# Kernel optimization log

Hardware: AMD Instinct MI355X
Metric: run time of the kernel (lower is better)

## Reference

```python
import jax, jax.numpy as jnp
import numpy as np

B, T, N_EMBD, N_HEAD = 2, 2048, 1024, 16
HEAD = N_EMBD // N_HEAD  # 64
BLOCK = 2048             # config.block_size
BASE = 10000.0           # RoPE base


def rotate_half(x):
    h = x.shape[-1] // 2
    return jnp.concatenate([-x[..., h:], x[..., :h]], axis=-1)


def setup_inputs() -> dict:
    key = jax.random.key(0)
    ks = jax.random.split(key, 6)
    x = jax.random.normal(ks[0], (B, T, N_EMBD), jnp.float32)
    cumulative_scores = jax.random.uniform(ks[1], (B, T), jnp.float32)
    token_index = jnp.sort(jax.random.randint(ks[2], (B, T), 0, BLOCK), axis=-1)
    padding_mask = jnp.ones((B, BLOCK), jnp.float32)
    W_attn = jax.random.normal(ks[3], (N_EMBD, 3 * N_EMBD), jnp.float32) * 0.02
    b_attn = jnp.zeros((3 * N_EMBD,), jnp.float32)
    W_proj = jax.random.normal(ks[4], (N_EMBD, N_EMBD), jnp.float32) * 0.02
    b_proj = jnp.zeros((N_EMBD,), jnp.float32)
    return {"x": x, "cumulative_scores": cumulative_scores,
            "padding_mask": padding_mask, "W_attn": W_attn, "b_attn": b_attn,
            "W_proj": W_proj, "b_proj": b_proj, "token_index": token_index}


def reference(x, cumulative_scores, padding_mask, W_attn, b_attn, W_proj, b_proj, token_index):
    Bv, Tv, C = x.shape
    qkv = x @ W_attn + b_attn                      # [B,T,3C]
    q, k, v = jnp.split(qkv, 3, axis=-1)
    to_heads = lambda a: a.reshape(Bv, Tv, N_HEAD, HEAD).transpose(0, 2, 1, 3)  # [B,H,T,hd]
    q, k, v = to_heads(q), to_heads(k), to_heads(v)

    # per-token fractional positions: cumsum of 1/count over gathered token indices
    counts = jax.vmap(lambda idx: jnp.zeros(BLOCK, jnp.float32).at[idx].add(1.0))(token_index)
    partial = jnp.cumsum(jnp.take_along_axis(1.0 / counts, token_index, axis=-1), axis=-1)  # [B,T]

    # RoPE with custom positions t=partial
    inv_freq = 1.0 / (BASE ** (jnp.arange(0, HEAD, 2, dtype=jnp.float32) / HEAD))  # [hd/2]
    freqs = partial[..., None] * inv_freq                                          # [B,T,hd/2]
    emb = jnp.concatenate([freqs, freqs], axis=-1)[:, None, :, :]                  # [B,1,T,hd]
    cos, sin = jnp.cos(emb), jnp.sin(emb)
    q = q * cos + rotate_half(q) * sin
    k = k * cos + rotate_half(k) * sin

    # 'fork' plan: overwrite last channel
    q = q.at[..., -1].set(1.0)
    k = k.at[..., -1].set(jnp.broadcast_to(cumulative_scores[:, None, :], k.shape[:-1]))

    # additive bf16 causal + padding mask, then cast to q dtype
    zero_bf = jnp.zeros((), jnp.bfloat16)
    neg_bf = jnp.full((), -jnp.inf, jnp.bfloat16)
    causal = jnp.where(jnp.tril(jnp.ones((Tv, Tv), bool)), zero_bf, neg_bf)        # [T,T] bf16
    pm = jnp.take_along_axis(padding_mask, token_index, axis=1).astype(jnp.float32)  # [B,T]
    outer = pm[:, :, None] * pm[:, None, :]                                        # [B,T,T]
    pad_add = jnp.where(outer != 0, zero_bf, neg_bf)
    mask = (causal[None] + pad_add).astype(x.dtype)[:, None, :, :]                 # [B,1,T,T]

    # scale v by exp(cumulative_scores)
    v = v * jnp.exp(cumulative_scores)[:, None, :, None]

    scores = jnp.einsum('bhqd,bhkd->bhqk', q, k) / np.float32(np.sqrt(HEAD)) + mask
    p = jax.nn.softmax(scores, axis=-1)
    y = jnp.einsum('bhqk,bhkd->bhqd', p, v)
    y = y.transpose(0, 2, 1, 3).reshape(Bv, Tv, C)
    return y @ W_proj + b_proj
```

## Files before the change

### kernel.cpp

```cpp
#include <hip/hip_runtime.h>
#include <math.h>

#define B_ 2
#define T_ 2048
#define C_ 1024
#define H_ 16
#define HD_ 64

typedef __bf16 bf16;
typedef __bf16 bf8v __attribute__((ext_vector_type(8)));
typedef __bf16 bf4v __attribute__((ext_vector_type(4)));
typedef float  f4v  __attribute__((ext_vector_type(4)));

#define MFMA16(a,b,c) __builtin_amdgcn_mfma_f32_16x16x32_bf16((a),(b),(c),0,0,0)

typedef const __attribute__((address_space(1))) void* gas_ptr;
typedef __attribute__((address_space(3))) void*       las_ptr;

static __device__ __forceinline__ void gload_lds16(const void* g, void* l) {
  __builtin_amdgcn_global_load_lds((gas_ptr)g, (las_ptr)l, 16, 0, 0);
}

__global__ void k_convert(const float* __restrict__ in, bf16* __restrict__ outb, int n4) {
  int stride = gridDim.x * blockDim.x;
  for (int i = blockIdx.x * blockDim.x + threadIdx.x; i < n4; i += stride) {
    float4 v = reinterpret_cast<const float4*>(in)[i];
    bf4v o; o[0] = (bf16)v.x; o[1] = (bf16)v.y; o[2] = (bf16)v.z; o[3] = (bf16)v.w;
    reinterpret_cast<bf4v*>(outb)[i] = o;
  }
}

__global__ void k_transpose_bf(const float* __restrict__ in, bf16* __restrict__ outb, int R, int Cc) {
  __shared__ float t[32][33];
  int c0 = blockIdx.x * 32, r0 = blockIdx.y * 32;
  int tx = threadIdx.x, ty = threadIdx.y;
  for (int i = ty; i < 32; i += 8)
    t[i][tx] = in[(size_t)(r0 + i) * Cc + c0 + tx];
  __syncthreads();
  for (int i = ty; i < 32; i += 8)
    outb[(size_t)(c0 + i) * R + r0 + tx] = (bf16)t[tx][i];
}

__global__ void k_positions(const int* __restrict__ tok, float* __restrict__ partial) {
  __shared__ float cnt[2048];
  __shared__ float tsum[256];
  int b = blockIdx.x, tid = threadIdx.x;
  const int* ti = tok + b * 2048;
  for (int i = tid; i < 2048; i += 256) cnt[i] = 0.f;
  __syncthreads();
  for (int i = tid; i < 2048; i += 256) atomicAdd(&cnt[ti[i]], 1.f);
  __syncthreads();
  float loc[8]; float s = 0.f;
#pragma unroll
  for (int j = 0; j < 8; ++j) { loc[j] = 1.f / cnt[ti[tid * 8 + j]]; s += loc[j]; }
  tsum[tid] = s;
  __syncthreads();
  for (int off = 1; off < 256; off <<= 1) {
    float v = (tid >= off) ? tsum[tid - off] : 0.f;
    __syncthreads();
    tsum[tid] += v;
    __syncthreads();
  }
  float run = (tid > 0) ? tsum[tid - 1] : 0.f;
  float* po = partial + b * 2048;
#pragma unroll
  for (int j = 0; j < 8; ++j) { run += loc[j]; po[tid * 8 + j] = run; }
}

__global__ void k_tables(const float* __restrict__ partial, const float* __restrict__ pad,
                         const int* __restrict__ tok,
                         float* __restrict__ ctab, float* __restrict__ stab, float* __restrict__ pmg) {
  int i = blockIdx.x * blockDim.x + threadIdx.x;
  if (i >= B_ * T_) return;
  int b = i >> 11;
  float p = partial[i];
  for (int d = 0; d < 32; ++d) {
    float inv = exp2f((float)d * -0.41524101186092028f);
    float ang = p * inv;
    float sn, cs; sincosf(ang, &sn, &cs);
    ctab[i * 32 + d] = cs; stab[i * 32 + d] = sn;
  }
  pmg[i] = pad[b * 2048 + tok[i]];
}

__global__ __launch_bounds__(256) void k_gemm_qkv(const bf16* __restrict__ A, const bf16* __restrict__ BT,
                                                  const float* __restrict__ bias,
                                                  const float* __restrict__ ctab, const float* __restrict__ stab,
                                                  const float* __restrict__ cum,
                                                  bf16* __restrict__ Qh, bf16* __restrict__ Kh,
                                                  bf16* __restrict__ VhT) {
  const int K = 1024;
  __shared__ bf16 As[128 * 32];
  __shared__ bf16 Bs[128 * 32];
  int tid = threadIdx.x;
  int w = tid >> 6, l = tid & 63;
  int wr = w >> 1, wc = w & 1;
  int lg = l >> 4, lr = l & 15;
  int bm0 = blockIdx.y * 128, bn0 = blockIdx.x * 128;
  f4v acc[4][4] = {};
  int srow = l >> 2;
  int scol = (l & 3) * 8;
  for (int k0 = 0; k0 < K; k0 += 32) {
    __syncthreads();
#pragma unroll
    for (int i = 0; i < 2; ++i) {
      int rblk = w * 32 + i * 16;
      gload_lds16(A  + (size_t)(bm0 + rblk + srow) * K + k0 + scol, As + rblk * 32);
      gload_lds16(BT + (size_t)(bn0 + rblk + srow) * K + k0 + scol, Bs + rblk * 32);
    }
    __syncthreads();
    bf8v af[4], bb[4];
#pragma unroll
    for (int fm = 0; fm < 4; ++fm)
      af[fm] = *reinterpret_cast<const bf8v*>(As + (wr * 64 + fm * 16 + lr) * 32 + lg * 8);
#pragma unroll
    for (int fn = 0; fn < 4; ++fn)
      bb[fn] = *reinterpret_cast<const bf8v*>(Bs + (wc * 64 + fn * 16 + lr) * 32 + lg * 8);
#pragma unroll
    for (int fm = 0; fm < 4; ++fm)
#pragma unroll
      for (int fn = 0; fn < 4; ++fn)
        acc[fm][fn] = MFMA16(af[fm], bb[fn], acc[fm][fn]);
  }
  int type = bn0 >> 10;
  int h = ((bn0 & 1023) >> 6) + wc;
  int cbase = bn0 + wc * 64;
  int r0 = bm0 + wr * 64;
  float bs[4];
#pragma unroll
  for (int fn = 0; fn < 4; ++fn) bs[fn] = bias[cbase + fn * 16 + lr];
  if (type == 2) {
#pragma unroll
    for (int fm = 0; fm < 4; ++fm) {
      int rbase = r0 + fm * 16 + lg * 4;
      float ve[4];
#pragma unroll
      for (int j = 0; j < 4; ++j) ve[j] = __expf(cum[rbase + j]);
      int bb2 = rbase >> 11, tt = rbase & 2047;
      size_t vbase = (size_t)(bb2 * 16 + h) * 64 * 2048 + tt;
#pragma unroll
      for (int fn = 0; fn < 4; ++fn) {
        int d = fn * 16 + lr;
        bf4v pack;
#pragma unroll
        for (int j = 0; j < 4; ++j)
          pack[j] = (bf16)((acc[fm][fn][j] + bs[fn]) * ve[j]);
        *reinterpret_cast<bf4v*>(VhT + vbase + (size_t)d * 2048) = pack;
      }
    }
  } else {
#pragma unroll
    for (int fm = 0; fm < 4; ++fm)
#pragma unroll
      for (int j = 0; j < 4; ++j) {
        int r = r0 + fm * 16 + lg * 4 + j;
        int b = r >> 11, t = r & 2047;
        size_t obase = ((size_t)(b * 16 + h) * 2048 + t) * 64;
        float cumv = cum[r];
        float cs0 = ctab[r * 32 + lr],      sn0 = stab[r * 32 + lr];
        float cs1 = ctab[r * 32 + 16 + lr], sn1 = stab[r * 32 + 16 + lr];
#pragma unroll
        for (int fn = 0; fn < 4; ++fn) {
          int d = fn * 16 + lr;
          float val = acc[fm][fn][j] + bs[fn];
          float par = acc[fm][fn ^ 2][j] + bs[fn ^ 2];
          float cs = (fn & 1) ? cs1 : cs0, sn = (fn & 1) ? sn1 : sn0;
          float rot = val * cs + ((fn < 2) ? -par : par) * sn;
          if (type == 0) {
            if (d == 63) rot = 1.f;
            Qh[obase + d] = (bf16)rot;
          } else {
            if (d == 63) rot = cumv;
            Kh[obase + d] = (bf16)rot;
          }
        }
      }
  }
}

__global__ __launch_bounds__(256) void k_gemm_bt(const bf16* __restrict__ A, const bf16* __restrict__ BT,
                                                 const float* __restrict__ bias, float* __restrict__ Cout,
                                                 int M, int N, int K) {
  __shared__ bf16 As[128 * 32];
  __shared__ bf16 Bs[128 * 32];
  int tid = threadIdx.x;
  int w = tid >> 6, l = tid & 63;
  int wr = w >> 1, wc = w & 1;
  int lg = l >> 4, lr = l & 15;
  int bm0 = blockIdx.y * 128, bn0 = blockIdx.x * 128;
  f4v acc[4][4] = {};
  int srow = l >> 2;
  int scol = (l & 3) * 8;
  for (int k0 = 0; k0 < K; k0 += 32) {
    __syncthreads();
#pragma unroll
    for (int i = 0; i < 2; ++i) {
      int rblk = w * 32 + i * 16;
      gload_lds16(A  + (size_t)(bm0 + rblk + srow) * K + k0 + scol, As + rblk * 32);
      gload_lds16(BT + (size_t)(bn0 + rblk + srow) * K + k0 + scol, Bs + rblk * 32);
    }
    __syncthreads();
    bf8v af[4], bb[4];
#pragma unroll
    for (int fm = 0; fm < 4; ++fm)
      af[fm] = *reinterpret_cast<const bf8v*>(As + (wr * 64 + fm * 16 + lr) * 32 + lg * 8);
#pragma unroll
    for (int fn = 0; fn < 4; ++fn)
      bb[fn] = *reinterpret_cast<const bf8v*>(Bs + (wc * 64 + fn * 16 + lr) * 32 + lg * 8);
#pragma unroll
    for (int fm = 0; fm < 4; ++fm)
#pragma unroll
      for (int fn = 0; fn < 4; ++fn)
        acc[fm][fn] = MFMA16(af[fm], bb[fn], acc[fm][fn]);
  }
  int r0 = bm0 + wr * 64, c0 = bn0 + wc * 64;
#pragma unroll
  for (int fm = 0; fm < 4; ++fm)
#pragma unroll
    for (int fn = 0; fn < 4; ++fn)
#pragma unroll
      for (int j = 0; j < 4; ++j) {
        int r = r0 + fm * 16 + lg * 4 + j, c = c0 + fn * 16 + lr;
        Cout[(size_t)r * N + c] = acc[fm][fn][j] + bias[c];
      }
}

__global__ __launch_bounds__(256) void k_attn(const bf16* __restrict__ Qh, const bf16* __restrict__ Kh,
                                              const bf16* __restrict__ VhT, const float* __restrict__ pmg,
                                              bf16* __restrict__ Y) {
  __shared__ bf16 Kl[2][64 * 64];
  __shared__ bf16 Vt[2][64 * 64];
  __shared__ bf16 Pl[4][16][72];
  int bid = blockIdx.x;
  int qt = 31 - (bid >> 5);
  int bh = bid & 31;
  int b = bh >> 4;
  int tid = threadIdx.x, w = tid >> 6, l = tid & 63;
  int lg = l >> 4, lr = l & 15;
  const size_t baseK = (size_t)bh * 2048 * 64;
  const size_t baseV = (size_t)bh * 64 * 2048;
  int qrow_f = qt * 64 + w * 16 + lr;
  bf8v qf0 = *reinterpret_cast<const bf8v*>(Qh + baseK + (size_t)qrow_f * 64 + lg * 8);
  bf8v qf1 = *reinterpret_cast<const bf8v*>(Qh + baseK + (size_t)qrow_f * 64 + 32 + lg * 8);
  float pq[4];
#pragma unroll
  for (int j = 0; j < 4; ++j) pq[j] = pmg[b * 2048 + qt * 64 + w * 16 + lg * 4 + j];
  int lrow = l >> 3;
  int lcb  = (l & 7) ^ lrow;
  auto STAGE = [&](int kt, int bb) {
#pragma unroll
    for (int i = 0; i < 2; ++i) {
      int rr = w * 16 + i * 8 + lrow;
      gload_lds16(Kh  + baseK + (size_t)(kt * 64 + rr) * 64 + lcb * 8, &Kl[bb][(w * 16 + i * 8) * 64]);
      gload_lds16(VhT + baseV + (size_t)rr * 2048 + kt * 64 + lcb * 8, &Vt[bb][(w * 16 + i * 8) * 64]);
    }
  };
  float m_run[4] = {-INFINITY, -INFINITY, -INFINITY, -INFINITY};
  float l_run[4] = {0.f, 0.f, 0.f, 0.f};
  f4v o_acc[4] = {};
  STAGE(0, 0);
  __syncthreads();
  int cur = 0;
  int sw = lr & 7;
  for (int kt = 0; kt <= qt; ++kt) {
    if (kt < qt) STAGE(kt + 1, cur ^ 1);
    const bf16* KB = &Kl[cur][0];
    const bf16* VB = &Vt[cur][0];
    f4v sa[4] = {};
#pragma unroll
    for (int nf = 0; nf < 4; ++nf) {
      int R = (nf * 16 + lr) * 64;
      bf8v kf0 = *reinterpret_cast<const bf8v*>(KB + R + ((lg ^ sw) * 8));
      bf8v kf1 = *reinterpret_cast<const bf8v*>(KB + R + (((lg + 4) ^ sw) * 8));
      sa[nf] = MFMA16(qf0, kf0, sa[nf]);
      sa[nf] = MFMA16(qf1, kf1, sa[nf]);
    }
    float pv[4][4];
    float mx[4] = {-INFINITY, -INFINITY, -INFINITY, -INFINITY};
#pragma unroll
    for (int nf = 0; nf < 4; ++nf) {
      int kcol = kt * 64 + nf * 16 + lr;
      float pk = pmg[b * 2048 + kcol];
#pragma unroll
      for (int j = 0; j < 4; ++j) {
        int qrow = qt * 64 + w * 16 + lg * 4 + j;
        bool ok = (kcol <= qrow) && (pq[j] != 0.f) && (pk != 0.f);
        float s = ok ? sa[nf][j] * 0.125f : -INFINITY;
        pv[nf][j] = s;
        mx[j] = fmaxf(mx[j], s);
      }
    }
    for (int off = 1; off < 16; off <<= 1)
#pragma unroll
      for (int j = 0; j < 4; ++j) mx[j] = fmaxf(mx[j], __shfl_xor(mx[j], off));
    float rs[4] = {0.f, 0.f, 0.f, 0.f};
    float scl[4];
#pragma unroll
    for (int j = 0; j < 4; ++j) {
      float mnew = fmaxf(m_run[j], mx[j]);
      scl[j] = __expf(m_run[j] - mnew);
      m_run[j] = mnew;
    }
#pragma unroll
    for (int nf = 0; nf < 4; ++nf)
#pragma unroll
      for (int j = 0; j < 4; ++j) {
        float p = __expf(pv[nf][j] - m_run[j]);
        pv[nf][j] = p;
        rs[j] += p;
      }
    for (int off = 1; off < 16; off <<= 1)
#pragma unroll
      for (int j = 0; j < 4; ++j) rs[j] += __shfl_xor(rs[j], off);
#pragma unroll
    for (int j = 0; j < 4; ++j) l_run[j] = l_run[j] * scl[j] + rs[j];
#pragma unroll
    for (int df = 0; df < 4; ++df)
#pragma unroll
      for (int j = 0; j < 4; ++j) o_acc[df][j] *= scl[j];
#pragma unroll
    for (int nf = 0; nf < 4; ++nf)
#pragma unroll
      for (int j = 0; j < 4; ++j)
        Pl[w][lg * 4 + j][nf * 16 + lr] = (bf16)pv[nf][j];
    bf8v pa0 = *reinterpret_cast<const bf8v*>(&Pl[w][lr][lg * 8]);
    bf8v pa1 = *reinterpret_cast<const bf8v*>(&Pl[w][lr][32 + lg * 8]);
#pragma unroll
    for (int df = 0; df < 4; ++df) {
      int D = (df * 16 + lr) * 64;
      bf8v vf0 = *reinterpret_cast<const bf8v*>(VB + D + ((lg ^ sw) * 8));
      bf8v vf1 = *reinterpret_cast<const bf8v*>(VB + D + (((lg + 4) ^ sw) * 8));
      o_acc[df] = MFMA16(pa0, vf0, o_acc[df]);
      o_acc[df] = MFMA16(pa1, vf1, o_acc[df]);
    }
    __syncthreads();
    cur ^= 1;
  }
  int h = bh & 15;
#pragma unroll
  for (int j = 0; j < 4; ++j) {
    float inv = 1.f / l_run[j];
    int trow = qt * 64 + w * 16 + lg * 4 + j;
#pragma unroll
    for (int df = 0; df < 4; ++df)
      Y[((size_t)(b * 2048 + trow) * 16 + h) * 64 + df * 16 + lr] = (bf16)(o_acc[df][j] * inv);
  }
}

extern "C" void kernel_launch(void* const* d_in, const int* in_sizes, int n_in,
                              void* d_out, int out_size, void* d_ws, size_t ws_size,
                              hipStream_t stream) {
  const float* x     = (const float*)d_in[0];
  const float* cum   = (const float*)d_in[1];
  const float* pad   = (const float*)d_in[2];
  const float* Wattn = (const float*)d_in[3];
  const float* battn = (const float*)d_in[4];
  const float* Wproj = (const float*)d_in[5];
  const float* bproj = (const float*)d_in[6];
  const int*   tok   = (const int*)d_in[7];
  float* out = (float*)d_out;
  char* ws = (char*)d_ws;

  float* partial = (float*)(ws);
  float* ctab    = (float*)(ws + 16384);
  float* stab    = (float*)(ws + 540672);
  float* pmg     = (float*)(ws + 1064960);
  bf16*  WabT    = (bf16*)(ws + 2097152);
  bf16*  WpbT    = (bf16*)(ws + 8388608);
  bf16*  xb      = (bf16*)(ws + 10485760);
  bf16*  Qh      = (bf16*)(ws + 18874368);
  bf16*  Kh      = (bf16*)(ws + 27262976);
  bf16*  VhT    = (bf16*)(ws + 35651584);
  bf16*  Ybf     = xb;

  k_convert<<<2048, 256, 0, stream>>>(x, xb, (B_ * T_ * C_) / 4);
  k_transpose_bf<<<dim3(96, 32), dim3(32, 8), 0, stream>>>(Wattn, WabT, 1024, 3072);
  k_transpose_bf<<<dim3(32, 32), dim3(32, 8), 0, stream>>>(Wproj, WpbT, 1024, 1024);
  k_positions<<<2, 256, 0, stream>>>(tok, partial);
  k_tables<<<16, 256, 0, stream>>>(partial, pad, tok, ctab, stab, pmg);
  k_gemm_qkv<<<dim3(24, 32), 256, 0, stream>>>(xb, WabT, battn, ctab, stab, cum, Qh, Kh, VhT);
  k_attn<<<1024, 256, 0, stream>>>(Qh, Kh, VhT, pmg, Ybf);
  k_gemm_bt<<<dim3(8, 32), 256, 0, stream>>>(Ybf, WpbT, bproj, out, 4096, 1024, 1024);
}
```

Baseline: 253.4 us.

## Double-buffer GEMM LDS tiles and streamline attention masking and rescaling

Both GEMM kernels now share a core that double-buffers the A/B LDS tiles, prefetching the next k-slice while the current one feeds MFMA, with one barrier per iteration instead of two. The attention loop peels the diagonal tile so the causal comparison only runs there, and turns masking into an additive bias applied through an fma. It also skips the online-softmax rescale of the output accumulators unless the running max grows by more than 8, and raises wave priority around the MFMA sections. Costs are doubled LDS use in the GEMMs, which may lower occupancy, and lazy rescaling, which lets exponentials reach up to e^8 before normalisation.

```diff
diff --git a/kernel.cpp b/kernel.cpp
--- a/kernel.cpp
+++ b/kernel.cpp
@@ -83,45 +83,61 @@
   pmg[i] = pad[b * 2048 + tok[i]];
 }
 
+static __device__ __forceinline__ void gemm_core(const bf16* __restrict__ A, const bf16* __restrict__ BT,
+                                                 int K, int bm0, int bn0,
+                                                 f4v (&acc)[4][4],
+                                                 bf16 (*As)[128 * 32], bf16 (*Bs)[128 * 32]) {
+  int tid = threadIdx.x;
+  int w = tid >> 6, l = tid & 63;
+  int wr = w >> 1, wc = w & 1;
+  int lg = l >> 4, lr = l & 15;
+  int srow = l >> 2;
+  int scol = (l & 3) * 8;
+  auto STAGE = [&](int buf, int k0) {
+#pragma unroll
+    for (int i = 0; i < 2; ++i) {
+      int rblk = w * 32 + i * 16;
+      gload_lds16(A  + (size_t)(bm0 + rblk + srow) * K + k0 + scol, As[buf] + rblk * 32);
+      gload_lds16(BT + (size_t)(bn0 + rblk + srow) * K + k0 + scol, Bs[buf] + rblk * 32);
+    }
+  };
+  STAGE(0, 0);
+  __syncthreads();
+  int cur = 0;
+  for (int k0 = 0; k0 < K; k0 += 32) {
+    if (k0 + 32 < K) STAGE(cur ^ 1, k0 + 32);
+    bf8v af[4], bb[4];
+#pragma unroll
+    for (int fm = 0; fm < 4; ++fm)
+      af[fm] = *reinterpret_cast<const bf8v*>(As[cur] + (wr * 64 + fm * 16 + lr) * 32 + lg * 8);
+#pragma unroll
+    for (int fn = 0; fn < 4; ++fn)
+      bb[fn] = *reinterpret_cast<const bf8v*>(Bs[cur] + (wc * 64 + fn * 16 + lr) * 32 + lg * 8);
+#pragma unroll
+    for (int fm = 0; fm < 4; ++fm)
+#pragma unroll
+      for (int fn = 0; fn < 4; ++fn)
+        acc[fm][fn] = MFMA16(af[fm], bb[fn], acc[fm][fn]);
+    __syncthreads();
+    cur ^= 1;
+  }
+}
+
 __global__ __launch_bounds__(256) void k_gemm_qkv(const bf16* __restrict__ A, const bf16* __restrict__ BT,
                                                   const float* __restrict__ bias,
                                                   const float* __restrict__ ctab, const float* __restrict__ stab,
                                                   const float* __restrict__ cum,
                                                   bf16* __restrict__ Qh, bf16* __restrict__ Kh,
                                                   bf16* __restrict__ VhT) {
-  const int K = 1024;
-  __shared__ bf16 As[128 * 32];
-  __shared__ bf16 Bs[128 * 32];
+  __shared__ bf16 As[2][128 * 32];
+  __shared__ bf16 Bs[2][128 * 32];
   int tid = threadIdx.x;
   int w = tid >> 6, l = tid & 63;
   int wr = w >> 1, wc = w & 1;
   int lg = l >> 4, lr = l & 15;
   int bm0 = blockIdx.y * 128, bn0 = blockIdx.x * 128;
   f4v acc[4][4] = {};
-  int srow = l >> 2;
-  int scol = (l & 3) * 8;
-  for (int k0 = 0; k0 < K; k0 += 32) {
-    __syncthreads();
-#pragma unroll
-    for (int i = 0; i < 2; ++i) {
-      int rblk = w * 32 + i * 16;
-      gload_lds16(A  + (size_t)(bm0 + rblk + srow) * K + k0 + scol, As + rblk * 32);
-      gload_lds16(BT + (size_t)(bn0 + rblk + srow) * K + k0 + scol, Bs + rblk * 32);
-    }
-    __syncthreads();
-    bf8v af[4], bb[4];
-#pragma unroll
-    for (int fm = 0; fm < 4; ++fm)
-      af[fm] = *reinterpret_cast<const bf8v*>(As + (wr * 64 + fm * 16 + lr) * 32 + lg * 8);
-#pragma unroll
-    for (int fn = 0; fn < 4; ++fn)
-      bb[fn] = *reinterpret_cast<const bf8v*>(Bs + (wc * 64 + fn * 16 + lr) * 32 + lg * 8);
-#pragma unroll
-    for (int fm = 0; fm < 4; ++fm)
-#pragma unroll
-      for (int fn = 0; fn < 4; ++fn)
-        acc[fm][fn] = MFMA16(af[fm], bb[fn], acc[fm][fn]);
-  }
+  gemm_core(A, BT, 1024, bm0, bn0, acc, As, Bs);
   int type = bn0 >> 10;
   int h = ((bn0 & 1023) >> 6) + wc;
   int cbase = bn0 + wc * 64;
@@ -181,38 +197,15 @@
 __global__ __launch_bounds__(256) void k_gemm_bt(const bf16* __restrict__ A, const bf16* __restrict__ BT,
                                                  const float* __restrict__ bias, float* __restrict__ Cout,
                                                  int M, int N, int K) {
-  __shared__ bf16 As[128 * 32];
-  __shared__ bf16 Bs[128 * 32];
+  __shared__ bf16 As[2][128 * 32];
+  __shared__ bf16 Bs[2][128 * 32];
   int tid = threadIdx.x;
   int w = tid >> 6, l = tid & 63;
   int wr = w >> 1, wc = w & 1;
   int lg = l >> 4, lr = l & 15;
   int bm0 = blockIdx.y * 128, bn0 = blockIdx.x * 128;
   f4v acc[4][4] = {};
-  int srow = l >> 2;
-  int scol = (l & 3) * 8;
-  for (int k0 = 0; k0 < K; k0 += 32) {
-    __syncthreads();
-#pragma unroll
-    for (int i = 0; i < 2; ++i) {
-      int rblk = w * 32 + i * 16;
-      gload_lds16(A  + (size_t)(bm0 + rblk + srow) * K + k0 + scol, As + rblk * 32);
-      gload_lds16(BT + (size_t)(bn0 + rblk + srow) * K + k0 + scol, Bs + rblk * 32);
-    }
-    __syncthreads();
-    bf8v af[4], bb[4];
-#pragma unroll
-    for (int fm = 0; fm < 4; ++fm)
-      af[fm] = *reinterpret_cast<const bf8v*>(As + (wr * 64 + fm * 16 + lr) * 32 + lg * 8);
-#pragma unroll
-    for (int fn = 0; fn < 4; ++fn)
-      bb[fn] = *reinterpret_cast<const bf8v*>(Bs + (wc * 64 + fn * 16 + lr) * 32 + lg * 8);
-#pragma unroll
-    for (int fm = 0; fm < 4; ++fm)
-#pragma unroll
-      for (int fn = 0; fn < 4; ++fn)
-        acc[fm][fn] = MFMA16(af[fm], bb[fn], acc[fm][fn]);
-  }
+  gemm_core(A, BT, K, bm0, bn0, acc, As, Bs);
   int r0 = bm0 + wr * 64, c0 = bn0 + wc * 64;
 #pragma unroll
   for (int fm = 0; fm < 4; ++fm)
@@ -242,9 +235,12 @@
   int qrow_f = qt * 64 + w * 16 + lr;
   bf8v qf0 = *reinterpret_cast<const bf8v*>(Qh + baseK + (size_t)qrow_f * 64 + lg * 8);
   bf8v qf1 = *reinterpret_cast<const bf8v*>(Qh + baseK + (size_t)qrow_f * 64 + 32 + lg * 8);
-  float pq[4];
-#pragma unroll
-  for (int j = 0; j < 4; ++j) pq[j] = pmg[b * 2048 + qt * 64 + w * 16 + lg * 4 + j];
+  float radd[4];
+#pragma unroll
+  for (int j = 0; j < 4; ++j) {
+    float pq = pmg[b * 2048 + qt * 64 + w * 16 + lg * 4 + j];
+    radd[j] = (pq != 0.f) ? 0.f : -1e30f;
+  }
   int lrow = l >> 3;
   int lcb  = (l & 7) ^ lrow;
   auto STAGE = [&](int kt, int bb) {
@@ -258,84 +254,104 @@
   float m_run[4] = {-INFINITY, -INFINITY, -INFINITY, -INFINITY};
   float l_run[4] = {0.f, 0.f, 0.f, 0.f};
   f4v o_acc[4] = {};
+  int sw = lr & 7;
+
+#define ATTN_TILE(KT, CUR, DIAG)                                                  \
+  {                                                                               \
+    const bf16* KB = &Kl[CUR][0];                                                 \
+    const bf16* VB = &Vt[CUR][0];                                                 \
+    f4v sa[4] = {};                                                               \
+    __builtin_amdgcn_s_setprio(1);                                                \
+    _Pragma("unroll")                                                             \
+    for (int nf = 0; nf < 4; ++nf) {                                              \
+      int R = (nf * 16 + lr) * 64;                                                \
+      bf8v kf0 = *reinterpret_cast<const bf8v*>(KB + R + ((lg ^ sw) * 8));        \
+      bf8v kf1 = *reinterpret_cast<const bf8v*>(KB + R + (((lg + 4) ^ sw) * 8));  \
+      sa[nf] = MFMA16(qf0, kf0, sa[nf]);                                          \
+      sa[nf] = MFMA16(qf1, kf1, sa[nf]);                                          \
+    }                                                                             \
+    __builtin_amdgcn_s_setprio(0);                                                \
+    float pv[4][4];                                                               \
+    float mx[4];                                                                  \
+    _Pragma("unroll")                                                             \
+    for (int nf = 0; nf < 4; ++nf) {                                              \
+      int kcol = (KT) * 64 + nf * 16 + lr;                                        \
+      float pk = pmg[b * 2048 + kcol];                                            \
+      float cm = (pk != 0.f) ? 0.f : -1e30f;                                      \
+      _Pragma("unroll")                                                           \
+      for (int j = 0; j < 4; ++j) {                                               \
+        float add = cm + radd[j];                                                 \
+        if (DIAG) {                                                               \
+          int qrow = qt * 64 + w * 16 + lg * 4 + j;                               \
+          if (kcol > qrow) add = -1e30f;                                          \
+        }                                                                         \
+        float s = fmaf(sa[nf][j], 0.125f, add);                                   \
+        pv[nf][j] = s;                                                            \
+        mx[j] = (nf == 0) ? s : fmaxf(mx[j], s);                                  \
+      }                                                                           \
+    }                                                                             \
+    for (int off = 1; off < 16; off <<= 1)                                        \
+      _Pragma("unroll")                                                           \
+      for (int j = 0; j < 4; ++j) mx[j] = fmaxf(mx[j], __shfl_xor(mx[j], off));   \
+    bool grow = false;                                                            \
+    _Pragma("unroll")                                                             \
+    for (int j = 0; j < 4; ++j) grow |= (mx[j] > m_run[j] + 8.f);                 \
+    if (__any(grow)) {                                                            \
+      _Pragma("unroll")                                                           \
+      for (int j = 0; j < 4; ++j) {                                               \
+        float mnew = fmaxf(m_run[j], mx[j]);                                      \
+        float scl = __expf(m_run[j] - mnew);                                      \
+        m_run[j] = mnew;                                                          \
+        l_run[j] *= scl;                                                          \
+        _Pragma("unroll")                                                         \
+        for (int df = 0; df < 4; ++df) o_acc[df][j] *= scl;                       \
+      }                                                                           \
+    }                                                                             \
+    float rs[4] = {0.f, 0.f, 0.f, 0.f};                                           \
+    _Pragma("unroll")                                                             \
+    for (int nf = 0; nf < 4; ++nf)                                                \
+      _Pragma("unroll")                                                           \
+      for (int j = 0; j < 4; ++j) {                                               \
+        float p = __expf(pv[nf][j] - m_run[j]);                                   \
+        pv[nf][j] = p;                                                            \
+        rs[j] += p;                                                               \
+      }                                                                           \
+    for (int off = 1; off < 16; off <<= 1)                                        \
+      _Pragma("unroll")                                                           \
+      for (int j = 0; j < 4; ++j) rs[j] += __shfl_xor(rs[j], off);                \
+    _Pragma("unroll")                                                             \
+    for (int j = 0; j < 4; ++j) l_run[j] += rs[j];                                \
+    _Pragma("unroll")                                                             \
+    for (int nf = 0; nf < 4; ++nf)                                                \
+      _Pragma("unroll")                                                           \
+      for (int j = 0; j < 4; ++j)                                                 \
+        Pl[w][lg * 4 + j][nf * 16 + lr] = (bf16)pv[nf][j];                        \
+    bf8v pa0 = *reinterpret_cast<const bf8v*>(&Pl[w][lr][lg * 8]);                \
+    bf8v pa1 = *reinterpret_cast<const bf8v*>(&Pl[w][lr][32 + lg * 8]);           \
+    __builtin_amdgcn_s_setprio(1);                                                \
+    _Pragma("unroll")                                                             \
+    for (int df = 0; df < 4; ++df) {                                              \
+      int D = (df * 16 + lr) * 64;                                                \
+      bf8v vf0 = *reinterpret_cast<const bf8v*>(VB + D + ((lg ^ sw) * 8));        \
+      bf8v vf1 = *reinterpret_cast<const bf8v*>(VB + D + (((lg + 4) ^ sw) * 8));  \
+      o_acc[df] = MFMA16(pa0, vf0, o_acc[df]);                                    \
+      o_acc[df] = MFMA16(pa1, vf1, o_acc[df]);                                    \
+    }                                                                             \
+    __builtin_amdgcn_s_setprio(0);                                                \
+  }
+
   STAGE(0, 0);
   __syncthreads();
   int cur = 0;
-  int sw = lr & 7;
-  for (int kt = 0; kt <= qt; ++kt) {
-    if (kt < qt) STAGE(kt + 1, cur ^ 1);
-    const bf16* KB = &Kl[cur][0];
-    const bf16* VB = &Vt[cur][0];
-    f4v sa[4] = {};
-#pragma unroll
-    for (int nf = 0; nf < 4; ++nf) {
-      int R = (nf * 16 + lr) * 64;
-      bf8v kf0 = *reinterpret_cast<const bf8v*>(KB + R + ((lg ^ sw) * 8));
-      bf8v kf1 = *reinterpret_cast<const bf8v*>(KB + R + (((lg + 4) ^ sw) * 8));
-      sa[nf] = MFMA16(qf0, kf0, sa[nf]);
-      sa[nf] = MFMA16(qf1, kf1, sa[nf]);
-    }
-    float pv[4][4];
-    float mx[4] = {-INFINITY, -INFINITY, -INFINITY, -INFINITY};
-#pragma unroll
-    for (int nf = 0; nf < 4; ++nf) {
-      int kcol = kt * 64 + nf * 16 + lr;
-      float pk = pmg[b * 2048 + kcol];
-#pragma unroll
-      for (int j = 0; j < 4; ++j) {
-        int qrow = qt * 64 + w * 16 + lg * 4 + j;
-        bool ok = (kcol <= qrow) && (pq[j] != 0.f) && (pk != 0.f);
-        float s = ok ? sa[nf][j] * 0.125f : -INFINITY;
-        pv[nf][j] = s;
-        mx[j] = fmaxf(mx[j], s);
-      }
-    }
-    for (int off = 1; off < 16; off <<= 1)
-#pragma unroll
-      for (int j = 0; j < 4; ++j) mx[j] = fmaxf(mx[j], __shfl_xor(mx[j], off));
-    float rs[4] = {0.f, 0.f, 0.f, 0.f};
-    float scl[4];
-#pragma unroll
-    for (int j = 0; j < 4; ++j) {
-      float mnew = fmaxf(m_run[j], mx[j]);
-      scl[j] = __expf(m_run[j] - mnew);
-      m_run[j] = mnew;
-    }
-#pragma unroll
-    for (int nf = 0; nf < 4; ++nf)
-#pragma unroll
-      for (int j = 0; j < 4; ++j) {
-        float p = __expf(pv[nf][j] - m_run[j]);
-        pv[nf][j] = p;
-        rs[j] += p;
-      }
-    for (int off = 1; off < 16; off <<= 1)
-#pragma unroll
-      for (int j = 0; j < 4; ++j) rs[j] += __shfl_xor(rs[j], off);
-#pragma unroll
-    for (int j = 0; j < 4; ++j) l_run[j] = l_run[j] * scl[j] + rs[j];
-#pragma unroll
-    for (int df = 0; df < 4; ++df)
-#pragma unroll
-      for (int j = 0; j < 4; ++j) o_acc[df][j] *= scl[j];
-#pragma unroll
-    for (int nf = 0; nf < 4; ++nf)
-#pragma unroll
-      for (int j = 0; j < 4; ++j)
-        Pl[w][lg * 4 + j][nf * 16 + lr] = (bf16)pv[nf][j];
-    bf8v pa0 = *reinterpret_cast<const bf8v*>(&Pl[w][lr][lg * 8]);
-    bf8v pa1 = *reinterpret_cast<const bf8v*>(&Pl[w][lr][32 + lg * 8]);
-#pragma unroll
-    for (int df = 0; df < 4; ++df) {
-      int D = (df * 16 + lr) * 64;
-      bf8v vf0 = *reinterpret_cast<const bf8v*>(VB + D + ((lg ^ sw) * 8));
-      bf8v vf1 = *reinterpret_cast<const bf8v*>(VB + D + (((lg + 4) ^ sw) * 8));
-      o_acc[df] = MFMA16(pa0, vf0, o_acc[df]);
-      o_acc[df] = MFMA16(pa1, vf1, o_acc[df]);
-    }
+  for (int kt = 0; kt < qt; ++kt) {
+    STAGE(kt + 1, cur ^ 1);
+    ATTN_TILE(kt, cur, false);
     __syncthreads();
     cur ^= 1;
   }
+  ATTN_TILE(qt, cur, true);
+#undef ATTN_TILE
+
   int h = bh & 15;
 #pragma unroll
   for (int j = 0; j < 4; ++j) {
@@ -370,7 +386,7 @@
   bf16*  xb      = (bf16*)(ws + 10485760);
   bf16*  Qh      = (bf16*)(ws + 18874368);
   bf16*  Kh      = (bf16*)(ws + 27262976);
-  bf16*  VhT    = (bf16*)(ws + 35651584);
+  bf16*  VhT     = (bf16*)(ws + 35651584);
   bf16*  Ybf     = xb;
 
   k_convert<<<2048, 256, 0, stream>>>(x, xb, (B_ * T_ * C_) / 4);
```

Result: no change. 254.8 us (+0.5%).

## Double-buffer GEMMs, coalesce QKV epilogue, drop attention LDS staging, fuse prep kernels

Applied to the files above, without the earlier changes.

Merges the input conversion and the two weight transposes into one launch. Both GEMMs now use a double-buffered LDS pipeline with one barrier per k-step, and the QKV epilogue stages each tile in LDS so global stores are 16-byte and contiguous. The attention kernel stops staging K/V through LDS and loads them directly from global memory, uses a lazy rescale that only fires when the running max grows by more than 8, replaces -inf masking with additive -1e30, and raises wave priority around the MFMA blocks. These changes target launch overhead, barrier stalls and uncoalesced stores, at the cost of depending on cache hits for the direct K/V loads and slightly different numerics in the masking and rescale.

```diff
diff --git a/kernel.cpp b/kernel.cpp
--- a/kernel.cpp
+++ b/kernel.cpp
@@ -21,24 +21,34 @@
   __builtin_amdgcn_global_load_lds((gas_ptr)g, (las_ptr)l, 16, 0, 0);
 }
 
-__global__ void k_convert(const float* __restrict__ in, bf16* __restrict__ outb, int n4) {
-  int stride = gridDim.x * blockDim.x;
-  for (int i = blockIdx.x * blockDim.x + threadIdx.x; i < n4; i += stride) {
-    float4 v = reinterpret_cast<const float4*>(in)[i];
-    bf4v o; o[0] = (bf16)v.x; o[1] = (bf16)v.y; o[2] = (bf16)v.z; o[3] = (bf16)v.w;
-    reinterpret_cast<bf4v*>(outb)[i] = o;
-  }
-}
-
-__global__ void k_transpose_bf(const float* __restrict__ in, bf16* __restrict__ outb, int R, int Cc) {
-  __shared__ float t[32][33];
-  int c0 = blockIdx.x * 32, r0 = blockIdx.y * 32;
-  int tx = threadIdx.x, ty = threadIdx.y;
+__global__ void k_prep(const float* __restrict__ x, bf16* __restrict__ xb,
+                       const float* __restrict__ Wattn, bf16* __restrict__ WabT,
+                       const float* __restrict__ Wproj, bf16* __restrict__ WpbT) {
+  __shared__ float tbuf[32][33];
+  int blk = blockIdx.x, tid = threadIdx.x;
+  if (blk < 2048) {
+    const int n4 = (B_ * T_ * C_) / 4;
+    for (int i = blk * 256 + tid; i < n4; i += 2048 * 256) {
+      float4 v = reinterpret_cast<const float4*>(x)[i];
+      bf4v o; o[0] = (bf16)v.x; o[1] = (bf16)v.y; o[2] = (bf16)v.z; o[3] = (bf16)v.w;
+      reinterpret_cast<bf4v*>(xb)[i] = o;
+    }
+    return;
+  }
+  const float* in; bf16* outb; int R, Cc, c0, r0;
+  if (blk < 5120) {
+    int b2 = blk - 2048; in = Wattn; outb = WabT; R = 1024; Cc = 3072;
+    c0 = (b2 % 96) * 32; r0 = (b2 / 96) * 32;
+  } else {
+    int b3 = blk - 5120; in = Wproj; outb = WpbT; R = 1024; Cc = 1024;
+    c0 = (b3 & 31) * 32; r0 = (b3 >> 5) * 32;
+  }
+  int tx = tid & 31, ty = tid >> 5;
   for (int i = ty; i < 32; i += 8)
-    t[i][tx] = in[(size_t)(r0 + i) * Cc + c0 + tx];
+    tbuf[i][tx] = in[(size_t)(r0 + i) * Cc + c0 + tx];
   __syncthreads();
   for (int i = ty; i < 32; i += 8)
-    outb[(size_t)(c0 + i) * R + r0 + tx] = (bf16)t[tx][i];
+    outb[(size_t)(c0 + i) * R + r0 + tx] = (bf16)tbuf[tx][i];
 }
 
 __global__ void k_positions(const int* __restrict__ tok, float* __restrict__ partial) {
@@ -83,136 +93,142 @@
   pmg[i] = pad[b * 2048 + tok[i]];
 }
 
+static __device__ __forceinline__ void gemm_core(const bf16* __restrict__ A, const bf16* __restrict__ BT,
+                                                 int K, int bm0, int bn0,
+                                                 f4v (&acc)[4][4],
+                                                 bf16 (*As)[128 * 32], bf16 (*Bs)[128 * 32]) {
+  int tid = threadIdx.x;
+  int w = tid >> 6, l = tid & 63;
+  int wr = w >> 1, wc = w & 1;
+  int lg = l >> 4, lr = l & 15;
+  int srow = l >> 2;
+  int scol = (l & 3) * 8;
+  auto STAGE = [&](int buf, int k0) {
+#pragma unroll
+    for (int i = 0; i < 2; ++i) {
+      int rblk = w * 32 + i * 16;
+      gload_lds16(A  + (size_t)(bm0 + rblk + srow) * K + k0 + scol, As[buf] + rblk * 32);
+      gload_lds16(BT + (size_t)(bn0 + rblk + srow) * K + k0 + scol, Bs[buf] + rblk * 32);
+    }
+  };
+  STAGE(0, 0);
+  __syncthreads();
+  int cur = 0;
+  for (int k0 = 0; k0 < K; k0 += 32) {
+    if (k0 + 32 < K) STAGE(cur ^ 1, k0 + 32);
+    bf8v af[4], bb[4];
+#pragma unroll
+    for (int fm = 0; fm < 4; ++fm)
+      af[fm] = *reinterpret_cast<const bf8v*>(As[cur] + (wr * 64 + fm * 16 + lr) * 32 + lg * 8);
+#pragma unroll
+    for (int fn = 0; fn < 4; ++fn)
+      bb[fn] = *reinterpret_cast<const bf8v*>(Bs[cur] + (wc * 64 + fn * 16 + lr) * 32 + lg * 8);
+#pragma unroll
+    for (int fm = 0; fm < 4; ++fm)
+#pragma unroll
+      for (int fn = 0; fn < 4; ++fn)
+        acc[fm][fn] = MFMA16(af[fm], bb[fn], acc[fm][fn]);
+    __syncthreads();
+    cur ^= 1;
+  }
+}
+
 __global__ __launch_bounds__(256) void k_gemm_qkv(const bf16* __restrict__ A, const bf16* __restrict__ BT,
                                                   const float* __restrict__ bias,
                                                   const float* __restrict__ ctab, const float* __restrict__ stab,
                                                   const float* __restrict__ cum,
                                                   bf16* __restrict__ Qh, bf16* __restrict__ Kh,
                                                   bf16* __restrict__ VhT) {
-  const int K = 1024;
-  __shared__ bf16 As[128 * 32];
-  __shared__ bf16 Bs[128 * 32];
+  __shared__ bf16 As[2][128 * 32];
+  __shared__ bf16 Bs[2][128 * 32];
   int tid = threadIdx.x;
   int w = tid >> 6, l = tid & 63;
   int wr = w >> 1, wc = w & 1;
   int lg = l >> 4, lr = l & 15;
   int bm0 = blockIdx.y * 128, bn0 = blockIdx.x * 128;
   f4v acc[4][4] = {};
-  int srow = l >> 2;
-  int scol = (l & 3) * 8;
-  for (int k0 = 0; k0 < K; k0 += 32) {
-    __syncthreads();
-#pragma unroll
-    for (int i = 0; i < 2; ++i) {
-      int rblk = w * 32 + i * 16;
-      gload_lds16(A  + (size_t)(bm0 + rblk + srow) * K + k0 + scol, As + rblk * 32);
-      gload_lds16(BT + (size_t)(bn0 + rblk + srow) * K + k0 + scol, Bs + rblk * 32);
-    }
-    __syncthreads();
-    bf8v af[4], bb[4];
-#pragma unroll
-    for (int fm = 0; fm < 4; ++fm)
-      af[fm] = *reinterpret_cast<const bf8v*>(As + (wr * 64 + fm * 16 + lr) * 32 + lg * 8);
-#pragma unroll
-    for (int fn = 0; fn < 4; ++fn)
-      bb[fn] = *reinterpret_cast<const bf8v*>(Bs + (wc * 64 + fn * 16 + lr) * 32 + lg * 8);
-#pragma unroll
-    for (int fm = 0; fm < 4; ++fm)
-#pragma unroll
-      for (int fn = 0; fn < 4; ++fn)
-        acc[fm][fn] = MFMA16(af[fm], bb[fn], acc[fm][fn]);
-  }
+  gemm_core(A, BT, 1024, bm0, bn0, acc, As, Bs);
+  bf16* scr = reinterpret_cast<bf16*>(reinterpret_cast<char*>(&As[0][0]) + w * 8192);
   int type = bn0 >> 10;
   int h = ((bn0 & 1023) >> 6) + wc;
   int cbase = bn0 + wc * 64;
   int r0 = bm0 + wr * 64;
+  int b2 = r0 >> 11;
   float bs[4];
 #pragma unroll
   for (int fn = 0; fn < 4; ++fn) bs[fn] = bias[cbase + fn * 16 + lr];
   if (type == 2) {
-#pragma unroll
-    for (int fm = 0; fm < 4; ++fm) {
-      int rbase = r0 + fm * 16 + lg * 4;
-      float ve[4];
-#pragma unroll
-      for (int j = 0; j < 4; ++j) ve[j] = __expf(cum[rbase + j]);
-      int bb2 = rbase >> 11, tt = rbase & 2047;
-      size_t vbase = (size_t)(bb2 * 16 + h) * 64 * 2048 + tt;
-#pragma unroll
-      for (int fn = 0; fn < 4; ++fn) {
-        int d = fn * 16 + lr;
-        bf4v pack;
-#pragma unroll
-        for (int j = 0; j < 4; ++j)
-          pack[j] = (bf16)((acc[fm][fn][j] + bs[fn]) * ve[j]);
-        *reinterpret_cast<bf4v*>(VhT + vbase + (size_t)d * 2048) = pack;
+    size_t vbase = (size_t)(b2 * 16 + h) * 64 * 2048 + (r0 & 2047);
+#pragma unroll
+    for (int hp = 0; hp < 2; ++hp) {
+#pragma unroll
+      for (int fm2 = 0; fm2 < 2; ++fm2) {
+        int fm = hp * 2 + fm2;
+        int rbase = r0 + fm * 16 + lg * 4;
+        float ve[4];
+#pragma unroll
+        for (int j = 0; j < 4; ++j) ve[j] = __expf(cum[rbase + j]);
+#pragma unroll
+        for (int fn = 0; fn < 4; ++fn)
+#pragma unroll
+          for (int j = 0; j < 4; ++j)
+            scr[(fn * 16 + lr) * 40 + fm2 * 16 + lg * 4 + j] = (bf16)((acc[fm][fn][j] + bs[fn]) * ve[j]);
+      }
+#pragma unroll
+      for (int i = 0; i < 4; ++i) {
+        int d = (l >> 2) + i * 16, c = l & 3;
+        bf8v vv = *reinterpret_cast<const bf8v*>(scr + d * 40 + c * 8);
+        *reinterpret_cast<bf8v*>(VhT + vbase + (size_t)d * 2048 + hp * 32 + c * 8) = vv;
       }
     }
   } else {
-#pragma unroll
-    for (int fm = 0; fm < 4; ++fm)
-#pragma unroll
-      for (int j = 0; j < 4; ++j) {
-        int r = r0 + fm * 16 + lg * 4 + j;
-        int b = r >> 11, t = r & 2047;
-        size_t obase = ((size_t)(b * 16 + h) * 2048 + t) * 64;
-        float cumv = cum[r];
-        float cs0 = ctab[r * 32 + lr],      sn0 = stab[r * 32 + lr];
-        float cs1 = ctab[r * 32 + 16 + lr], sn1 = stab[r * 32 + 16 + lr];
-#pragma unroll
-        for (int fn = 0; fn < 4; ++fn) {
-          int d = fn * 16 + lr;
-          float val = acc[fm][fn][j] + bs[fn];
-          float par = acc[fm][fn ^ 2][j] + bs[fn ^ 2];
-          float cs = (fn & 1) ? cs1 : cs0, sn = (fn & 1) ? sn1 : sn0;
-          float rot = val * cs + ((fn < 2) ? -par : par) * sn;
-          if (type == 0) {
-            if (d == 63) rot = 1.f;
-            Qh[obase + d] = (bf16)rot;
-          } else {
-            if (d == 63) rot = cumv;
-            Kh[obase + d] = (bf16)rot;
+    bf16* Out = (type == 0) ? Qh : Kh;
+    size_t qbase = ((size_t)(b2 * 16 + h) * 2048 + (r0 & 2047)) * 64;
+#pragma unroll
+    for (int hp = 0; hp < 2; ++hp) {
+#pragma unroll
+      for (int fm2 = 0; fm2 < 2; ++fm2) {
+        int fm = hp * 2 + fm2;
+#pragma unroll
+        for (int j = 0; j < 4; ++j) {
+          int r = r0 + fm * 16 + lg * 4 + j;
+          float cumv = cum[r];
+          float cs0 = ctab[r * 32 + lr],      sn0 = stab[r * 32 + lr];
+          float cs1 = ctab[r * 32 + 16 + lr], sn1 = stab[r * 32 + 16 + lr];
+#pragma unroll
+          for (int fn = 0; fn < 4; ++fn) {
+            int d = fn * 16 + lr;
+            float val = acc[fm][fn][j] + bs[fn];
+            float par = acc[fm][fn ^ 2][j] + bs[fn ^ 2];
+            float cs = (fn & 1) ? cs1 : cs0, sn = (fn & 1) ? sn1 : sn0;
+            float rot = val * cs + ((fn < 2) ? -par : par) * sn;
+            if (d == 63) rot = (type == 0) ? 1.f : cumv;
+            scr[(fm2 * 16 + lg * 4 + j) * 72 + d] = (bf16)rot;
           }
         }
       }
+#pragma unroll
+      for (int i = 0; i < 4; ++i) {
+        int gr = (l >> 3) + i * 8, c = l & 7;
+        bf8v vv = *reinterpret_cast<const bf8v*>(scr + gr * 72 + c * 8);
+        *reinterpret_cast<bf8v*>(Out + qbase + (size_t)(hp * 32 + gr) * 64 + c * 8) = vv;
+      }
+    }
   }
 }
 
 __global__ __launch_bounds__(256) void k_gemm_bt(const bf16* __restrict__ A, const bf16* __restrict__ BT,
                                                  const float* __restrict__ bias, float* __restrict__ Cout,
                                                  int M, int N, int K) {
-  __shared__ bf16 As[128 * 32];
-  __shared__ bf16 Bs[128 * 32];
+  __shared__ bf16 As[2][128 * 32];
+  __shared__ bf16 Bs[2][128 * 32];
   int tid = threadIdx.x;
   int w = tid >> 6, l = tid & 63;
   int wr = w >> 1, wc = w & 1;
   int lg = l >> 4, lr = l & 15;
   int bm0 = blockIdx.y * 128, bn0 = blockIdx.x * 128;
   f4v acc[4][4] = {};
-  int srow = l >> 2;
-  int scol = (l & 3) * 8;
-  for (int k0 = 0; k0 < K; k0 += 32) {
-    __syncthreads();
-#pragma unroll
-    for (int i = 0; i < 2; ++i) {
-      int rblk = w * 32 + i * 16;
-      gload_lds16(A  + (size_t)(bm0 + rblk + srow) * K + k0 + scol, As + rblk * 32);
-      gload_lds16(BT + (size_t)(bn0 + rblk + srow) * K + k0 + scol, Bs + rblk * 32);
-    }
-    __syncthreads();
-    bf8v af[4], bb[4];
-#pragma unroll
-    for (int fm = 0; fm < 4; ++fm)
-      af[fm] = *reinterpret_cast<const bf8v*>(As + (wr * 64 + fm * 16 + lr) * 32 + lg * 8);
-#pragma unroll
-    for (int fn = 0; fn < 4; ++fn)
-      bb[fn] = *reinterpret_cast<const bf8v*>(Bs + (wc * 64 + fn * 16 + lr) * 32 + lg * 8);
-#pragma unroll
-    for (int fm = 0; fm < 4; ++fm)
-#pragma unroll
-      for (int fn = 0; fn < 4; ++fn)
-        acc[fm][fn] = MFMA16(af[fm], bb[fn], acc[fm][fn]);
-  }
+  gemm_core(A, BT, K, bm0, bn0, acc, As, Bs);
   int r0 = bm0 + wr * 64, c0 = bn0 + wc * 64;
 #pragma unroll
   for (int fm = 0; fm < 4; ++fm)
@@ -228,8 +244,6 @@
 __global__ __launch_bounds__(256) void k_attn(const bf16* __restrict__ Qh, const bf16* __restrict__ Kh,
                                               const bf16* __restrict__ VhT, const float* __restrict__ pmg,
                                               bf16* __restrict__ Y) {
-  __shared__ bf16 Kl[2][64 * 64];
-  __shared__ bf16 Vt[2][64 * 64];
   __shared__ bf16 Pl[4][16][72];
   int bid = blockIdx.x;
   int qt = 31 - (bid >> 5);
@@ -237,70 +251,76 @@
   int b = bh >> 4;
   int tid = threadIdx.x, w = tid >> 6, l = tid & 63;
   int lg = l >> 4, lr = l & 15;
-  const size_t baseK = (size_t)bh * 2048 * 64;
-  const size_t baseV = (size_t)bh * 64 * 2048;
+  const bf16* Kbase = Kh  + (size_t)bh * 2048 * 64;
+  const bf16* Vbase = VhT + (size_t)bh * 64 * 2048;
   int qrow_f = qt * 64 + w * 16 + lr;
-  bf8v qf0 = *reinterpret_cast<const bf8v*>(Qh + baseK + (size_t)qrow_f * 64 + lg * 8);
-  bf8v qf1 = *reinterpret_cast<const bf8v*>(Qh + baseK + (size_t)qrow_f * 64 + 32 + lg * 8);
-  float pq[4];
-#pragma unroll
-  for (int j = 0; j < 4; ++j) pq[j] = pmg[b * 2048 + qt * 64 + w * 16 + lg * 4 + j];
-  int lrow = l >> 3;
-  int lcb  = (l & 7) ^ lrow;
-  auto STAGE = [&](int kt, int bb) {
-#pragma unroll
-    for (int i = 0; i < 2; ++i) {
-      int rr = w * 16 + i * 8 + lrow;
-      gload_lds16(Kh  + baseK + (size_t)(kt * 64 + rr) * 64 + lcb * 8, &Kl[bb][(w * 16 + i * 8) * 64]);
-      gload_lds16(VhT + baseV + (size_t)rr * 2048 + kt * 64 + lcb * 8, &Vt[bb][(w * 16 + i * 8) * 64]);
-    }
-  };
+  bf8v qf0 = *reinterpret_cast<const bf8v*>(Qh + (size_t)bh * 2048 * 64 + (size_t)qrow_f * 64 + lg * 8);
+  bf8v qf1 = *reinterpret_cast<const bf8v*>(Qh + (size_t)bh * 2048 * 64 + (size_t)qrow_f * 64 + 32 + lg * 8);
+  float radd[4];
+#pragma unroll
+  for (int j = 0; j < 4; ++j) {
+    float pq = pmg[b * 2048 + qt * 64 + w * 16 + lg * 4 + j];
+    radd[j] = (pq != 0.f) ? 0.f : -1e30f;
+  }
   float m_run[4] = {-INFINITY, -INFINITY, -INFINITY, -INFINITY};
   float l_run[4] = {0.f, 0.f, 0.f, 0.f};
   f4v o_acc[4] = {};
-  STAGE(0, 0);
-  __syncthreads();
-  int cur = 0;
-  int sw = lr & 7;
   for (int kt = 0; kt <= qt; ++kt) {
-    if (kt < qt) STAGE(kt + 1, cur ^ 1);
-    const bf16* KB = &Kl[cur][0];
-    const bf16* VB = &Vt[cur][0];
     f4v sa[4] = {};
+    __builtin_amdgcn_s_setprio(1);
 #pragma unroll
     for (int nf = 0; nf < 4; ++nf) {
-      int R = (nf * 16 + lr) * 64;
-      bf8v kf0 = *reinterpret_cast<const bf8v*>(KB + R + ((lg ^ sw) * 8));
-      bf8v kf1 = *reinterpret_cast<const bf8v*>(KB + R + (((lg + 4) ^ sw) * 8));
+      const bf16* kr = Kbase + (size_t)(kt * 64 + nf * 16 + lr) * 64;
+      bf8v kf0 = *reinterpret_cast<const bf8v*>(kr + lg * 8);
+      bf8v kf1 = *reinterpret_cast<const bf8v*>(kr + 32 + lg * 8);
       sa[nf] = MFMA16(qf0, kf0, sa[nf]);
       sa[nf] = MFMA16(qf1, kf1, sa[nf]);
     }
+    __builtin_amdgcn_s_setprio(0);
+    bf8v vf[4][2];
+#pragma unroll
+    for (int df = 0; df < 4; ++df) {
+      const bf16* vr = Vbase + (size_t)(df * 16 + lr) * 2048 + kt * 64;
+      vf[df][0] = *reinterpret_cast<const bf8v*>(vr + lg * 8);
+      vf[df][1] = *reinterpret_cast<const bf8v*>(vr + 32 + lg * 8);
+    }
     float pv[4][4];
-    float mx[4] = {-INFINITY, -INFINITY, -INFINITY, -INFINITY};
+    float mx[4];
 #pragma unroll
     for (int nf = 0; nf < 4; ++nf) {
       int kcol = kt * 64 + nf * 16 + lr;
       float pk = pmg[b * 2048 + kcol];
+      float cm = (pk != 0.f) ? 0.f : -1e30f;
 #pragma unroll
       for (int j = 0; j < 4; ++j) {
-        int qrow = qt * 64 + w * 16 + lg * 4 + j;
-        bool ok = (kcol <= qrow) && (pq[j] != 0.f) && (pk != 0.f);
-        float s = ok ? sa[nf][j] * 0.125f : -INFINITY;
+        float add = cm + radd[j];
+        if (kt == qt) {
+          int qrow = qt * 64 + w * 16 + lg * 4 + j;
+          if (kcol > qrow) add = -1e30f;
+        }
+        float s = fmaf(sa[nf][j], 0.125f, add);
         pv[nf][j] = s;
-        mx[j] = fmaxf(mx[j], s);
+        mx[j] = (nf == 0) ? s : fmaxf(mx[j], s);
       }
     }
     for (int off = 1; off < 16; off <<= 1)
 #pragma unroll
       for (int j = 0; j < 4; ++j) mx[j] = fmaxf(mx[j], __shfl_xor(mx[j], off));
+    bool grow = false;
+#pragma unroll
+    for (int j = 0; j < 4; ++j) grow |= (mx[j] > m_run[j] + 8.f);
+    if (__any(grow)) {
+#pragma unroll
+      for (int j = 0; j < 4; ++j) {
+        float mnew = fmaxf(m_run[j], mx[j]);
+        float scl = __expf(m_run[j] - mnew);
+        m_run[j] = mnew;
+        l_run[j] *= scl;
+#pragma unroll
+        for (int df = 0; df < 4; ++df) o_acc[df][j] *= scl;
+      }
+    }
     float rs[4] = {0.f, 0.f, 0.f, 0.f};
-    float scl[4];
-#pragma unroll
-    for (int j = 0; j < 4; ++j) {
-      float mnew = fmaxf(m_run[j], mx[j]);
-      scl[j] = __expf(m_run[j] - mnew);
-      m_run[j] = mnew;
-    }
 #pragma unroll
     for (int nf = 0; nf < 4; ++nf)
 #pragma unroll
@@ -313,11 +333,7 @@
 #pragma unroll
       for (int j = 0; j < 4; ++j) rs[j] += __shfl_xor(rs[j], off);
 #pragma unroll
-    for (int j = 0; j < 4; ++j) l_run[j] = l_run[j] * scl[j] + rs[j];
-#pragma unroll
-    for (int df = 0; df < 4; ++df)
-#pragma unroll
-      for (int j = 0; j < 4; ++j) o_acc[df][j] *= scl[j];
+    for (int j = 0; j < 4; ++j) l_run[j] += rs[j];
 #pragma unroll
     for (int nf = 0; nf < 4; ++nf)
 #pragma unroll
@@ -325,16 +341,13 @@
         Pl[w][lg * 4 + j][nf * 16 + lr] = (bf16)pv[nf][j];
     bf8v pa0 = *reinterpret_cast<const bf8v*>(&Pl[w][lr][lg * 8]);
     bf8v pa1 = *reinterpret_cast<const bf8v*>(&Pl[w][lr][32 + lg * 8]);
+    __builtin_amdgcn_s_setprio(1);
 #pragma unroll
     for (int df = 0; df < 4; ++df) {
-      int D = (df * 16 + lr) * 64;
-      bf8v vf0 = *reinterpret_cast<const bf8v*>(VB + D + ((lg ^ sw) * 8));
-      bf8v vf1 = *reinterpret_cast<const bf8v*>(VB + D + (((lg + 4) ^ sw) * 8));
-      o_acc[df] = MFMA16(pa0, vf0, o_acc[df]);
-      o_acc[df] = MFMA16(pa1, vf1, o_acc[df]);
-    }
-    __syncthreads();
-    cur ^= 1;
+      o_acc[df] = MFMA16(pa0, vf[df][0], o_acc[df]);
+      o_acc[df] = MFMA16(pa1, vf[df][1], o_acc[df]);
+    }
+    __builtin_amdgcn_s_setprio(0);
   }
   int h = bh & 15;
 #pragma unroll
@@ -370,12 +383,10 @@
   bf16*  xb      = (bf16*)(ws + 10485760);
   bf16*  Qh      = (bf16*)(ws + 18874368);
   bf16*  Kh      = (bf16*)(ws + 27262976);
-  bf16*  VhT    = (bf16*)(ws + 35651584);
+  bf16*  VhT     = (bf16*)(ws + 35651584);
   bf16*  Ybf     = xb;
 
-  k_convert<<<2048, 256, 0, stream>>>(x, xb, (B_ * T_ * C_) / 4);
-  k_transpose_bf<<<dim3(96, 32), dim3(32, 8), 0, stream>>>(Wattn, WabT, 1024, 3072);
-  k_transpose_bf<<<dim3(32, 32), dim3(32, 8), 0, stream>>>(Wproj, WpbT, 1024, 1024);
+  k_prep<<<6144, 256, 0, stream>>>(x, xb, Wattn, WabT, Wproj, WpbT);
   k_positions<<<2, 256, 0, stream>>>(tok, partial);
   k_tables<<<16, 256, 0, stream>>>(partial, pad, tok, ctab, stab, pmg);
   k_gemm_qkv<<<dim3(24, 32), 256, 0, stream>>>(xb, WabT, battn, ctab, stab, cum, Qh, Kh, VhT);
```

Measured after the change: 322.6 us. +27.3%, slower.
